# Optimization experiments

Hardware: AMD Instinct MI355X
Metric: run time of the kernel (lower is better)

Reference implementation:

```python
import jax, jax.numpy as jnp
import numpy as np

C_S, C_Z, C_H, H, PQ, PV = 384, 128, 16, 12, 4, 8
B, N = 1, 512
W_C = (2.0 / (9.0 * PQ)) ** 0.5
W_L = (1.0 / 3.0) ** 0.5
OUT_IN = H * C_Z + H * C_H + H * PV * 3 + H * PV  # 2112


def setup_inputs() -> dict:
    key = jax.random.key(0)
    ks = jax.random.split(key, 16)
    s_i = jax.random.normal(ks[0], (B, N, C_S), jnp.float32)
    z_ij = jax.random.normal(ks[1], (B, N, N, C_Z), jnp.float32)
    # random rotation matrices via QR
    raw = jax.random.normal(ks[2], (B, N, 3, 3), jnp.float32)
    q, r = jnp.linalg.qr(raw)
    rots = q * jnp.sign(jnp.diagonal(r, axis1=-2, axis2=-1))[..., None, :]
    trans = jax.random.normal(ks[3], (B, N, 3), jnp.float32)
    sc = lambda fan_in: 1.0 / np.sqrt(fan_in)
    Wq = jax.random.normal(ks[4], (C_S, H * C_H), jnp.float32) * sc(C_S)
    Wk = jax.random.normal(ks[5], (C_S, H * C_H), jnp.float32) * sc(C_S)
    Wv = jax.random.normal(ks[6], (C_S, H * C_H), jnp.float32) * sc(C_S)
    Wqp = jax.random.normal(ks[7], (C_S, H * PQ * 3), jnp.float32) * sc(C_S)
    Wkp = jax.random.normal(ks[8], (C_S, H * PQ * 3), jnp.float32) * sc(C_S)
    Wvp = jax.random.normal(ks[9], (C_S, H * PV * 3), jnp.float32) * sc(C_S)
    Wb = jax.random.normal(ks[10], (C_Z, H), jnp.float32) * sc(C_Z)
    gamma = jax.random.normal(ks[11], (1, 1, 1, H), jnp.float32)
    Wout = jax.random.normal(ks[12], (OUT_IN, C_S), jnp.float32) * sc(OUT_IN)
    bout = jnp.zeros((C_S,), jnp.float32)
    return dict(s_i=s_i, z_ij=z_ij, rots=rots, trans=trans, Wq=Wq, Wk=Wk, Wv=Wv,
                Wqp=Wqp, Wkp=Wkp, Wvp=Wvp, Wb=Wb, gamma=gamma, Wout=Wout, bout=bout)


def reference(s_i, z_ij, rots, trans, Wq, Wk, Wv, Wqp, Wkp, Wvp, Wb, gamma, Wout, bout):
    b, n = s_i.shape[0], s_i.shape[1]
    q_h = (s_i @ Wq).reshape(b, n, H, C_H)
    k_h = (s_i @ Wk).reshape(b, n, H, C_H)
    v_h = (s_i @ Wv).reshape(b, n, H, C_H)
    q_hp = (s_i @ Wqp).reshape(b, n, H, PQ, 3)
    k_hp = (s_i @ Wkp).reshape(b, n, H, PQ, 3)
    v_hp = (s_i @ Wvp).reshape(b, n, H, PV, 3)
    b_ij = z_ij @ Wb  # (b,i,j,h)

    t = trans[:, :, None, None, :]  # (b,i,1,1,3)
    apply = lambda x: jnp.einsum('bixy,bihpy->bihpx', rots, x) + t
    inv_apply = lambda x: jnp.einsum('bixy,bihpx->bihpy', rots, x - t)

    qg = apply(q_hp)  # (b,i,h,p,3) global frame
    kg = apply(k_hp)
    # pairwise rigid point distance term: (b,i,j,h)
    diff = qg[:, :, None] - kg[:, None]  # (b,i,j,h,p,3)
    dist2 = jnp.sum(diff * diff, axis=(-1, -2))

    a_s = jnp.einsum('bihd,bjhd->bijh', q_h, k_h) / (C_H ** 0.5)
    a_rigid = (W_C / 2.0) * gamma * dist2
    a = jax.nn.softmax(W_L * (a_s + b_ij - a_rigid), axis=-2)  # softmax over j

    o_hat = jnp.einsum('bijh,bijd->bihd', a, z_ij)
    o = jnp.einsum('bijh,bjhd->bihd', a, v_h)
    vg = apply(v_hp)  # (b,j,h,p,3)
    o_hp = inv_apply(jnp.einsum('bijh,bjhpx->bihpx', a, vg))  # (b,i,h,pv,3)
    o_hp_norm = jnp.sqrt(jnp.sum(o_hp * o_hp, axis=-1))  # (b,i,h,pv)

    cat = jnp.concatenate([
        o_hat.reshape(b, n, H * C_Z),
        o.reshape(b, n, H * C_H),
        o_hp.reshape(b, n, H * PV * 3),
        o_hp_norm.reshape(b, n, H * PV),
    ], axis=-1)
    return cat @ Wout + bout
```

## Files before the change

kernel.cpp:

```cpp
#include <hip/hip_runtime.h>
#include <hip/hip_bf16.h>
#include <math.h>

#define NRES 512
#define CS   384
#define CZ   128
#define NH   12
#define PW   1152
#define JB   64
#define NCH  8
#define PSTRIDE32 1040
#define KS   6
#define KAW  352

static constexpr float WL_F      = 0.57735026918962576f;
static constexpr float HALF_WC_F = 0.11785113019775792f;

typedef __attribute__((ext_vector_type(8))) short short8v;
typedef __attribute__((ext_vector_type(4))) float floatx4;

__device__ __forceinline__ ushort f2b(float f) {
    union { float f; uint u; } v; v.f = f;
    return (ushort)((v.u + 0x7FFFu + ((v.u >> 16) & 1u)) >> 16);
}
__device__ __forceinline__ float b2f(ushort b) {
    union { uint u; float f; } v; v.u = ((uint)b) << 16; return v.f;
}

__global__ __launch_bounds__(256) void k_prep(
    const float* __restrict__ Wq, const float* __restrict__ Wk,
    const float* __restrict__ Wv, const float* __restrict__ Wqp,
    const float* __restrict__ Wkp, const float* __restrict__ Wvp,
    const float* __restrict__ Wb, const float* __restrict__ Wout,
    float* __restrict__ Wcat, ushort* __restrict__ wbt16,
    ushort* __restrict__ woT)
{
    __shared__ ushort tile[64][72];
    const int bx = blockIdx.x;
    if (bx < 384) {
        const int c = bx;
        for (int col = threadIdx.x; col < PW; col += 256) {
            float v;
            if (col < 192)      v = Wq [(size_t)c * 192 + col];
            else if (col < 384) v = Wk [(size_t)c * 192 + col - 192];
            else if (col < 576) v = Wv [(size_t)c * 192 + col - 384];
            else if (col < 720) v = Wqp[(size_t)c * 144 + col - 576];
            else if (col < 864) v = Wkp[(size_t)c * 144 + col - 720];
            else                v = Wvp[(size_t)c * 288 + col - 864];
            Wcat[(size_t)c * PW + col] = v;
        }
        if (bx == 0) {
            for (int idx = threadIdx.x; idx < 16 * 128; idx += 256) {
                const int h = idx >> 7, cc = idx & 127;
                wbt16[idx] = (h < NH) ? f2b(WL_F * Wb[(size_t)cc * NH + h]) : (ushort)0;
            }
        }
    } else {
        const int t = bx - 384;
        const int k0 = (t % 33) * 64, c0 = (t / 33) * 64;
        for (int idx = threadIdx.x; idx < 4096; idx += 256) {
            const int r = idx >> 6, c = idx & 63;
            tile[r][c] = f2b(Wout[(size_t)(k0 + r) * 384 + c0 + c]);
        }
        __syncthreads();
        for (int idx = threadIdx.x; idx < 4096; idx += 256) {
            const int c = idx >> 6, r = idx & 63;
            woT[(size_t)(c0 + c) * 2112 + k0 + r] = tile[r][c];
        }
    }
}

__global__ __launch_bounds__(256) void k_gemm(
    const float* __restrict__ s, const float* __restrict__ Wcat,
    const float* __restrict__ rots, const float* __restrict__ trans,
    float* __restrict__ P)
{
    const int tid = threadIdx.x;
    const int tx = tid & 15, ty = tid >> 4;
    const int n0 = blockIdx.x * 48;
    const int m0 = blockIdx.y * 32;
    __shared__ float As[32][34];
    __shared__ float Bs[32][50];
    __shared__ float rot_lds[32][12];

    if (n0 >= 576) {
        for (int idx = tid; idx < 32 * 12; idx += 256) {
            int r = idx / 12, q = idx % 12;
            rot_lds[r][q] = (q < 9) ? rots[(size_t)(m0 + r) * 9 + q]
                                    : trans[(size_t)(m0 + r) * 3 + q - 9];
        }
    }

    float acc[2][3];
    #pragma unroll
    for (int u = 0; u < 2; ++u)
        #pragma unroll
        for (int v = 0; v < 3; ++v) acc[u][v] = 0.f;

    for (int k0 = 0; k0 < CS; k0 += 32) {
        __syncthreads();
        #pragma unroll
        for (int l = 0; l < 4; ++l) {
            int idx = tid + l * 256;
            int kk = idx & 31, r = idx >> 5;
            As[kk][r] = s[(size_t)(m0 + r) * CS + k0 + kk];
        }
        #pragma unroll
        for (int l = 0; l < 6; ++l) {
            int idx = tid + l * 256;
            int kk = idx / 48, cc = idx % 48;
            Bs[kk][cc] = Wcat[(size_t)(k0 + kk) * PW + n0 + cc];
        }
        __syncthreads();
        #pragma unroll
        for (int kk = 0; kk < 32; ++kk) {
            const float2 a = *(const float2*)&As[kk][ty * 2];
            const float b0 = Bs[kk][tx * 3], b1 = Bs[kk][tx * 3 + 1], b2 = Bs[kk][tx * 3 + 2];
            acc[0][0] += a.x * b0; acc[0][1] += a.x * b1; acc[0][2] += a.x * b2;
            acc[1][0] += a.y * b0; acc[1][1] += a.y * b1; acc[1][2] += a.y * b2;
        }
    }

    #pragma unroll
    for (int u = 0; u < 2; ++u) {
        float v0 = acc[u][0], v1 = acc[u][1], v2 = acc[u][2];
        if (n0 >= 576) {
            const float* RT = rot_lds[ty * 2 + u];
            const float p0 = v0, p1 = v1, p2 = v2;
            v0 = RT[0] * p0 + RT[1] * p1 + RT[2] * p2 + RT[9];
            v1 = RT[3] * p0 + RT[4] * p1 + RT[5] * p2 + RT[10];
            v2 = RT[6] * p0 + RT[7] * p1 + RT[8] * p2 + RT[11];
        }
        float* dst = P + (size_t)(m0 + ty * 2 + u) * PW + n0 + tx * 3;
        dst[0] = v0; dst[1] = v1; dst[2] = v2;
    }
}

__global__ __launch_bounds__(128) void k_ka(
    const float* __restrict__ P, ushort* __restrict__ Kfull)
{
    const int j = blockIdx.x;
    const int tid = threadIdx.x;
    __shared__ float njs[NH];
    const float* kr  = P + (size_t)j * PW + 192;
    const float* kgr = P + (size_t)j * PW + 720;
    if (tid < NH) {
        float s = 0.f;
        #pragma unroll
        for (int e = 0; e < 12; ++e) { const float v = kgr[tid * 12 + e]; s += v * v; }
        njs[tid] = s;
    }
    __syncthreads();
    ushort* dst = Kfull + (size_t)j * KAW;
    for (int t = tid; t < KAW; t += 128) {
        float v;
        if (t < 192)       v = kr[t];
        else if (t < 336)  v = kgr[t - 192];
        else if (t < 348)  v = njs[t - 336];
        else if (t == 348) v = 1.0f;
        else               v = 0.f;
        dst[t] = f2b(v);
    }
}

__global__ __launch_bounds__(256, 6) void k_flash(
    const float* __restrict__ z, const ushort* __restrict__ wbt16,
    const float* __restrict__ gamma, const float* __restrict__ P,
    const ushort* __restrict__ Kfull, uint* __restrict__ part)
{
    const int i   = blockIdx.x;
    const int jc  = blockIdx.y;
    const int j0  = jc * JB;
    const int tid = threadIdx.x;
    const int wid = tid >> 6, lane = tid & 63;

    __shared__ __align__(16) short zbT[128 * JB];
    __shared__ __align__(16) char  uni[10240];
    __shared__ float pm[NH], ps[NH];

    short*  BfT     = (short*)uni;
    float*  ltf     = (float*)uni;
    short*  ltb     = (short*)(uni + 4352);
    float4* halfacc = (float4*)(uni + 6400);

    uint* pb32   = part + ((size_t)i * NCH + jc) * PSTRIDE32;
    ushort* pb16 = (ushort*)pb32;
    float* pbf   = (float*)pb32;

    const int jb = wid * 16 + (lane & 15);
    const int ko = (lane >> 4) * 8;

    short8v af[4];
    {
        const float* za = z + ((size_t)i * NRES + j0 + jb) * CZ + ko;
        #pragma unroll
        for (int m = 0; m < 4; ++m) {
            const float4 f0 = *(const float4*)(za + m * 32);
            const float4 f1 = *(const float4*)(za + m * 32 + 4);
            short8v a;
            a[0] = (short)f2b(f0.x); a[1] = (short)f2b(f0.y);
            a[2] = (short)f2b(f0.z); a[3] = (short)f2b(f0.w);
            a[4] = (short)f2b(f1.x); a[5] = (short)f2b(f1.y);
            a[6] = (short)f2b(f1.z); a[7] = (short)f2b(f1.w);
            af[m] = a;
            #pragma unroll
            for (int e = 0; e < 8; ++e) {
                const int c = ko + m * 32 + e;
                zbT[c * 64 + (((jb >> 3) ^ (c & 7)) * 8) + (jb & 7)] = a[e];
            }
        }
    }
    {
        const float* prow = P + (size_t)i * PW;
        for (int t = tid; t < 12 * 352; t += 256) {
            const int h = t / 352, k = t - h * 352;
            float v = 0.f;
            if (k < 192) {
                if ((k >> 4) == h) v = 0.25f * WL_F * prow[k];
            } else if (k < 336) {
                const int e = k - 192;
                if (e / 12 == h) v = 2.f * HALF_WC_F * WL_F * gamma[h] * prow[576 + e];
            } else if (k < 348) {
                if (k - 336 == h) v = -HALF_WC_F * WL_F * gamma[h];
            } else if (k == 348) {
                float ss = 0.f;
                #pragma unroll
                for (int e = 0; e < 12; ++e) {
                    const float x = prow[576 + h * 12 + e];
                    ss += x * x;
                }
                v = -HALF_WC_F * WL_F * gamma[h] * ss;
            }
            BfT[t] = (short)f2b(v);
        }
    }
    __syncthreads();

    floatx4 lacc = {0.f, 0.f, 0.f, 0.f};
    {
        const int n  = lane & 15;
        const int nb = (n < NH) ? n : 0;
        const ushort* arow = Kfull + (size_t)(j0 + jb) * KAW + ko;
        const short*  brow = &BfT[nb * 352 + ko];
        const ushort* wrow = wbt16 + n * 128 + ko;
        #pragma unroll
        for (int st = 0; st < 11; ++st) {
            const short8v a = *(const short8v*)(arow + st * 32);
            const short8v b = *(const short8v*)(brow + st * 32);
            lacc = __builtin_amdgcn_mfma_f32_16x16x32_bf16(a, b, lacc, 0, 0, 0);
        }
        #pragma unroll
        for (int st = 0; st < 4; ++st) {
            const short8v b = *(const short8v*)(wrow + st * 32);
            lacc = __builtin_amdgcn_mfma_f32_16x16x32_bf16(af[st], b, lacc, 0, 0, 0);
        }
    }
    __syncthreads();
    {
        const int n = lane & 15;
        #pragma unroll
        for (int r = 0; r < 4; ++r)
            ltf[n * 68 + wid * 16 + (lane >> 4) * 4 + r] = lacc[r];
    }
    __syncthreads();

    if (tid < 192) {
        const int h = tid >> 4, s = tid & 15;
        float4 v = *(const float4*)&ltf[h * 68 + s * 4];
        float m = fmaxf(fmaxf(v.x, v.y), fmaxf(v.z, v.w));
        #pragma unroll
        for (int o = 1; o < 16; o <<= 1) m = fmaxf(m, __shfl_xor(m, o));
        float4 e;
        e.x = __expf(v.x - m); e.y = __expf(v.y - m);
        e.z = __expf(v.z - m); e.w = __expf(v.w - m);
        float sum = e.x + e.y + e.z + e.w;
        #pragma unroll
        for (int o = 1; o < 16; o <<= 1) sum += __shfl_xor(sum, o);
        *(float4*)&ltf[h * 68 + s * 4] = e;
        const uint lo = (uint)f2b(e.x) | ((uint)f2b(e.y) << 16);
        const uint hi = (uint)f2b(e.z) | ((uint)f2b(e.w) << 16);
        uint* dst = (uint*)&ltb[h * 64 + (((s >> 1) ^ (h & 7)) * 8) + (s & 1) * 4];
        dst[0] = lo; dst[1] = hi;
        if (s == 0) { pm[h] = m; ps[h] = sum; }
    } else {
        const int tt = tid - 192;
        uint* dst = (uint*)&ltb[(12 + (tt >> 4)) * 64 + (tt & 15) * 4];
        dst[0] = 0u; dst[1] = 0u;
    }
    __syncthreads();

    {
        const int hrow = lane & 15;
        const int u0 = (lane >> 4), u1 = u0 + 4;
        const short8v a0 = *(const short8v*)&ltb[hrow * 64 + ((u0 ^ (hrow & 7)) * 8)];
        const short8v a1 = *(const short8v*)&ltb[hrow * 64 + ((u1 ^ (hrow & 7)) * 8)];
        #pragma unroll
        for (int t = 0; t < 2; ++t) {
            const int d = (wid * 2 + t) * 16 + (lane & 15);
            const short8v b0 = *(const short8v*)&zbT[d * 64 + ((u0 ^ (d & 7)) * 8)];
            const short8v b1 = *(const short8v*)&zbT[d * 64 + ((u1 ^ (d & 7)) * 8)];
            floatx4 acc = {0.f, 0.f, 0.f, 0.f};
            acc = __builtin_amdgcn_mfma_f32_16x16x32_bf16(a0, b0, acc, 0, 0, 0);
            acc = __builtin_amdgcn_mfma_f32_16x16x32_bf16(a1, b1, acc, 0, 0, 0);
            #pragma unroll
            for (int r = 0; r < 4; ++r) {
                const int h = u0 * 4 + r;
                if (h < NH) pb16[h * 128 + d] = f2b(acc[r]);
            }
        }
    }

    {
        if (tid < 240) {
            const int half = tid / 120, col = tid % 120;
            int h;
            const float* base;
            if (col < 48) { h = col >> 2;               base = P + (size_t)j0 * PW + 384 + col * 4; }
            else          { const int cc = col - 48; h = cc / 6; base = P + (size_t)j0 * PW + 864 + cc * 4; }
            base += (size_t)(half * 32) * PW;
            const float* er = &ltf[h * 68 + half * 32];
            float ax = 0.f, ay = 0.f, az = 0.f, aw = 0.f;
            #pragma unroll 4
            for (int jj = 0; jj < 32; ++jj) {
                const float e = er[jj];
                const float4 v = *(const float4*)(base + (size_t)jj * PW);
                ax += e * v.x; ay += e * v.y; az += e * v.z; aw += e * v.w;
            }
            halfacc[tid] = make_float4(ax, ay, az, aw);
        }
        __syncthreads();
        if (tid < 120) {
            const float4 s0 = halfacc[tid], s1 = halfacc[tid + 120];
            const int off16 = (tid < 48) ? 1536 + tid * 4 : 1728 + (tid - 48) * 4;
            uint* dst = (uint*)&pb16[off16];
            dst[0] = (uint)f2b(s0.x + s1.x) | ((uint)f2b(s0.y + s1.y) << 16);
            dst[1] = (uint)f2b(s0.z + s1.z) | ((uint)f2b(s0.w + s1.w) << 16);
        }
        if (tid < NH) { pbf[1008 + tid] = pm[tid]; pbf[1020 + tid] = ps[tid]; }
    }
}

__global__ __launch_bounds__(256) void k_combine(
    const uint* __restrict__ part, const float* __restrict__ rots,
    const float* __restrict__ trans, ushort* __restrict__ cat16)
{
    const int i   = blockIdx.x;
    const int tid = threadIdx.x;
    __shared__ float wgt[NCH][NH];
    __shared__ float ohp[288];

    const uint* base = part + (size_t)i * NCH * PSTRIDE32;
    if (tid < NH) {
        const int h = tid;
        float mm[NCH];
        float M = -1e30f;
        #pragma unroll
        for (int c = 0; c < NCH; ++c) {
            mm[c] = ((const float*)(base + c * PSTRIDE32))[1008 + h];
            M = fmaxf(M, mm[c]);
        }
        float S = 0.f;
        #pragma unroll
        for (int c = 0; c < NCH; ++c) {
            const float w = __expf(mm[c] - M);
            S += w * ((const float*)(base + c * PSTRIDE32))[1020 + h];
            wgt[c][h] = w;
        }
        const float inv = 1.0f / S;
        #pragma unroll
        for (int c = 0; c < NCH; ++c) wgt[c][h] *= inv;
    }
    __syncthreads();

    ushort* crow = cat16 + (size_t)i * 2112;
    uint*   crowu = (uint*)crow;
    for (int idx2 = tid; idx2 < 768; idx2 += 256) {
        const int h = idx2 >> 6;
        float v0 = 0.f, v1 = 0.f;
        #pragma unroll
        for (int c = 0; c < NCH; ++c) {
            const uint u = base[c * PSTRIDE32 + idx2];
            const float w = wgt[c][h];
            v0 += b2f((ushort)u) * w;
            v1 += b2f((ushort)(u >> 16)) * w;
        }
        crowu[idx2] = (uint)f2b(v0) | ((uint)f2b(v1) << 16);
    }
    if (tid < 96) {
        const int h = tid >> 3;
        float v0 = 0.f, v1 = 0.f;
        #pragma unroll
        for (int c = 0; c < NCH; ++c) {
            const uint u = base[c * PSTRIDE32 + 768 + tid];
            const float w = wgt[c][h];
            v0 += b2f((ushort)u) * w;
            v1 += b2f((ushort)(u >> 16)) * w;
        }
        crowu[768 + tid] = (uint)f2b(v0) | ((uint)f2b(v1) << 16);
    }
    if (tid < 144) {
        const int h = tid / 12;
        float v0 = 0.f, v1 = 0.f;
        #pragma unroll
        for (int c = 0; c < NCH; ++c) {
            const uint u = base[c * PSTRIDE32 + 864 + tid];
            const float w = wgt[c][h];
            v0 += b2f((ushort)u) * w;
            v1 += b2f((ushort)(u >> 16)) * w;
        }
        ohp[tid * 2] = v0; ohp[tid * 2 + 1] = v1;
    }
    __syncthreads();

    if (tid < 96) {
        const int h = tid >> 3, p = tid & 7;
        float R[9];
        #pragma unroll
        for (int k = 0; k < 9; ++k) R[k] = rots[(size_t)i * 9 + k];
        const float g0 = ohp[h * 24 + p * 3 + 0] - trans[(size_t)i * 3 + 0];
        const float g1 = ohp[h * 24 + p * 3 + 1] - trans[(size_t)i * 3 + 1];
        const float g2 = ohp[h * 24 + p * 3 + 2] - trans[(size_t)i * 3 + 2];
        const float oy0 = R[0] * g0 + R[3] * g1 + R[6] * g2;
        const float oy1 = R[1] * g0 + R[4] * g1 + R[7] * g2;
        const float oy2 = R[2] * g0 + R[5] * g1 + R[8] * g2;
        crow[1728 + h * 24 + p * 3 + 0] = f2b(oy0);
        crow[1728 + h * 24 + p * 3 + 1] = f2b(oy1);
        crow[1728 + h * 24 + p * 3 + 2] = f2b(oy2);
        crow[2016 + h * 8 + p] = f2b(sqrtf(oy0 * oy0 + oy1 * oy1 + oy2 * oy2));
    }
}

__global__ __launch_bounds__(256) void k_out(
    const ushort* __restrict__ cat16, const ushort* __restrict__ woT,
    float* __restrict__ opart)
{
    const int tid = threadIdx.x;
    const int wid = tid >> 6, lane = tid & 63;
    const int wm = wid >> 1, wn = wid & 1;
    const int i0 = blockIdx.x * 32 + wm * 16;
    const int c0 = blockIdx.y * 32 + wn * 16;
    const int k0 = blockIdx.z * 352;
    const ushort* arow = cat16 + (size_t)(i0 + (lane & 15)) * 2112 + k0 + (lane >> 4) * 8;
    const ushort* brow = woT   + (size_t)(c0 + (lane & 15)) * 2112 + k0 + (lane >> 4) * 8;
    floatx4 acc = {0.f, 0.f, 0.f, 0.f};
    #pragma unroll
    for (int st = 0; st < 11; ++st) {
        const short8v a = *(const short8v*)(arow + st * 32);
        const short8v b = *(const short8v*)(brow + st * 32);
        acc = __builtin_amdgcn_mfma_f32_16x16x32_bf16(a, b, acc, 0, 0, 0);
    }
    float* ob = opart + (size_t)blockIdx.z * 512 * 384;
    #pragma unroll
    for (int r = 0; r < 4; ++r) {
        const int i = i0 + (lane >> 4) * 4 + r;
        ob[(size_t)i * 384 + c0 + (lane & 15)] = acc[r];
    }
}

__global__ __launch_bounds__(256) void k_outred(
    const float* __restrict__ opart, const float* __restrict__ bout,
    float* __restrict__ out)
{
    const int e4 = blockIdx.x * 256 + threadIdx.x;
    const float4* p = (const float4*)opart;
    const float4 b = ((const float4*)bout)[e4 % 96];
    float4 r = b;
    #pragma unroll
    for (int k = 0; k < KS; ++k) {
        const float4 v = p[e4 + k * 49152];
        r.x += v.x; r.y += v.y; r.z += v.z; r.w += v.w;
    }
    ((float4*)out)[e4] = r;
}

extern "C" void kernel_launch(void* const* d_in, const int* in_sizes, int n_in,
                              void* d_out, int out_size, void* d_ws, size_t ws_size,
                              hipStream_t stream)
{
    const float* s_i   = (const float*)d_in[0];
    const float* z_ij  = (const float*)d_in[1];
    const float* rots  = (const float*)d_in[2];
    const float* trans = (const float*)d_in[3];
    const float* Wq    = (const float*)d_in[4];
    const float* Wk    = (const float*)d_in[5];
    const float* Wv    = (const float*)d_in[6];
    const float* Wqp   = (const float*)d_in[7];
    const float* Wkp   = (const float*)d_in[8];
    const float* Wvp   = (const float*)d_in[9];
    const float* Wb    = (const float*)d_in[10];
    const float* gamma = (const float*)d_in[11];
    const float* Wout  = (const float*)d_in[12];
    const float* bout  = (const float*)d_in[13];
    float* ws = (float*)d_ws;
    float*  wcat  = ws;
    float*  P     = ws + 442368;
    uint*   part  = (uint*)(P + 589824);
    float*  opart = (float*)part;
    ushort* cat16 = (ushort*)(part + (size_t)512 * NCH * PSTRIDE32);
    ushort* wbt16 = cat16 + 1081344;
    ushort* kfull = wbt16 + 2048;
    ushort* woT   = kfull + 512 * KAW;
    float*  out   = (float*)d_out;

    hipLaunchKernelGGL(k_prep, dim3(582), dim3(256), 0, stream,
                       Wq, Wk, Wv, Wqp, Wkp, Wvp, Wb, Wout, wcat, wbt16, woT);
    hipLaunchKernelGGL(k_gemm, dim3(24, 16), dim3(256), 0, stream,
                       s_i, wcat, rots, trans, P);
    hipLaunchKernelGGL(k_ka, dim3(512), dim3(128), 0, stream, P, kfull);
    hipLaunchKernelGGL(k_flash, dim3(512, NCH), dim3(256), 0, stream,
                       z_ij, wbt16, gamma, P, kfull, part);
    hipLaunchKernelGGL(k_combine, dim3(512), dim3(256), 0, stream,
                       part, rots, trans, cat16);
    hipLaunchKernelGGL(k_out, dim3(16, 12, KS), dim3(256), 0, stream,
                       cat16, woT, opart);
    hipLaunchKernelGGL(k_outred, dim3(192), dim3(256), 0, stream,
                       opart, bout, out);
}
```

Before: 125.3 us.

## Precompute per-row query B-matrix in k_ka and shrink k_flash LDS footprint

The per-residue query operand (BfT, 12x352 bf16), which was rebuilt in LDS by each of the 8 j-chunk blocks of k_flash, is now built once per row in k_ka and written to a global Bfull buffer. k_flash reads B fragments straight from global memory, drops the BfT staging loop and one barrier, reuses zbT as scratch for halfacc, writes softmax max and sum directly to the partials, and raises the launch-bounds occupancy hint from 6 to 7. Bfull shares workspace with cat16, which is written later by k_combine. In exchange k_flash does more global (likely cache-hit) loads, and the lower LDS use is meant to allow more resident blocks.

```diff
diff --git a/kernel.cpp b/kernel.cpp
--- a/kernel.cpp
+++ b/kernel.cpp
@@ -12,6 +12,7 @@
 #define PSTRIDE32 1040
 #define KS   6
 #define KAW  352
+#define BFW  4224
 
 static constexpr float WL_F      = 0.57735026918962576f;
 static constexpr float HALF_WC_F = 0.11785113019775792f;
@@ -137,21 +138,28 @@
 }
 
 __global__ __launch_bounds__(128) void k_ka(
-    const float* __restrict__ P, ushort* __restrict__ Kfull)
-{
-    const int j = blockIdx.x;
+    const float* __restrict__ P, const float* __restrict__ gamma,
+    ushort* __restrict__ Kfull, ushort* __restrict__ Bfull)
+{
+    const int r = blockIdx.x;
     const int tid = threadIdx.x;
     __shared__ float njs[NH];
-    const float* kr  = P + (size_t)j * PW + 192;
-    const float* kgr = P + (size_t)j * PW + 720;
+    __shared__ float nqs[NH];
+    const float* prow = P + (size_t)r * PW;
+    const float* kr   = prow + 192;
+    const float* qgr  = prow + 576;
+    const float* kgr  = prow + 720;
     if (tid < NH) {
-        float s = 0.f;
-        #pragma unroll
-        for (int e = 0; e < 12; ++e) { const float v = kgr[tid * 12 + e]; s += v * v; }
-        njs[tid] = s;
+        float s = 0.f, sq = 0.f;
+        #pragma unroll
+        for (int e = 0; e < 12; ++e) {
+            const float v = kgr[tid * 12 + e];  s += v * v;
+            const float q = qgr[tid * 12 + e];  sq += q * q;
+        }
+        njs[tid] = s; nqs[tid] = sq;
     }
     __syncthreads();
-    ushort* dst = Kfull + (size_t)j * KAW;
+    ushort* dst = Kfull + (size_t)r * KAW;
     for (int t = tid; t < KAW; t += 128) {
         float v;
         if (t < 192)       v = kr[t];
@@ -161,12 +169,28 @@
         else               v = 0.f;
         dst[t] = f2b(v);
     }
-}
-
-__global__ __launch_bounds__(256, 6) void k_flash(
+    ushort* bd = Bfull + (size_t)r * BFW;
+    for (int t = tid; t < BFW; t += 128) {
+        const int h = t / 352, k = t - h * 352;
+        float v = 0.f;
+        if (k < 192) {
+            if ((k >> 4) == h) v = 0.25f * WL_F * prow[k];
+        } else if (k < 336) {
+            const int e = k - 192;
+            if (e / 12 == h) v = 2.f * HALF_WC_F * WL_F * gamma[h] * qgr[e];
+        } else if (k < 348) {
+            if (k - 336 == h) v = -HALF_WC_F * WL_F * gamma[h];
+        } else if (k == 348) {
+            v = -HALF_WC_F * WL_F * gamma[h] * nqs[h];
+        }
+        bd[t] = f2b(v);
+    }
+}
+
+__global__ __launch_bounds__(256, 7) void k_flash(
     const float* __restrict__ z, const ushort* __restrict__ wbt16,
-    const float* __restrict__ gamma, const float* __restrict__ P,
-    const ushort* __restrict__ Kfull, uint* __restrict__ part)
+    const float* __restrict__ P, const ushort* __restrict__ Kfull,
+    const ushort* __restrict__ Bfull, uint* __restrict__ part)
 {
     const int i   = blockIdx.x;
     const int jc  = blockIdx.y;
@@ -175,13 +199,9 @@
     const int wid = tid >> 6, lane = tid & 63;
 
     __shared__ __align__(16) short zbT[128 * JB];
-    __shared__ __align__(16) char  uni[10240];
-    __shared__ float pm[NH], ps[NH];
-
-    short*  BfT     = (short*)uni;
-    float*  ltf     = (float*)uni;
-    short*  ltb     = (short*)(uni + 4352);
-    float4* halfacc = (float4*)(uni + 6400);
+    __shared__ __align__(16) float ltf[12 * 68];
+    __shared__ __align__(16) short ltb[16 * 64];
+    float4* halfacc = (float4*)zbT;
 
     uint* pb32   = part + ((size_t)i * NCH + jc) * PSTRIDE32;
     ushort* pb16 = (ushort*)pb32;
@@ -210,39 +230,14 @@
             }
         }
     }
-    {
-        const float* prow = P + (size_t)i * PW;
-        for (int t = tid; t < 12 * 352; t += 256) {
-            const int h = t / 352, k = t - h * 352;
-            float v = 0.f;
-            if (k < 192) {
-                if ((k >> 4) == h) v = 0.25f * WL_F * prow[k];
-            } else if (k < 336) {
-                const int e = k - 192;
-                if (e / 12 == h) v = 2.f * HALF_WC_F * WL_F * gamma[h] * prow[576 + e];
-            } else if (k < 348) {
-                if (k - 336 == h) v = -HALF_WC_F * WL_F * gamma[h];
-            } else if (k == 348) {
-                float ss = 0.f;
-                #pragma unroll
-                for (int e = 0; e < 12; ++e) {
-                    const float x = prow[576 + h * 12 + e];
-                    ss += x * x;
-                }
-                v = -HALF_WC_F * WL_F * gamma[h] * ss;
-            }
-            BfT[t] = (short)f2b(v);
-        }
-    }
-    __syncthreads();
-
-    floatx4 lacc = {0.f, 0.f, 0.f, 0.f};
+
     {
         const int n  = lane & 15;
         const int nb = (n < NH) ? n : 0;
         const ushort* arow = Kfull + (size_t)(j0 + jb) * KAW + ko;
-        const short*  brow = &BfT[nb * 352 + ko];
+        const ushort* brow = Bfull + (size_t)i * BFW + nb * 352 + ko;
         const ushort* wrow = wbt16 + n * 128 + ko;
+        floatx4 lacc = {0.f, 0.f, 0.f, 0.f};
         #pragma unroll
         for (int st = 0; st < 11; ++st) {
             const short8v a = *(const short8v*)(arow + st * 32);
@@ -254,13 +249,11 @@
             const short8v b = *(const short8v*)(wrow + st * 32);
             lacc = __builtin_amdgcn_mfma_f32_16x16x32_bf16(af[st], b, lacc, 0, 0, 0);
         }
-    }
-    __syncthreads();
-    {
-        const int n = lane & 15;
-        #pragma unroll
-        for (int r = 0; r < 4; ++r)
-            ltf[n * 68 + wid * 16 + (lane >> 4) * 4 + r] = lacc[r];
+        if (n < NH) {
+            #pragma unroll
+            for (int r = 0; r < 4; ++r)
+                ltf[n * 68 + wid * 16 + (lane >> 4) * 4 + r] = lacc[r];
+        }
     }
     __syncthreads();
 
@@ -281,7 +274,7 @@
         const uint hi = (uint)f2b(e.z) | ((uint)f2b(e.w) << 16);
         uint* dst = (uint*)&ltb[h * 64 + (((s >> 1) ^ (h & 7)) * 8) + (s & 1) * 4];
         dst[0] = lo; dst[1] = hi;
-        if (s == 0) { pm[h] = m; ps[h] = sum; }
+        if (s == 0) { pbf[1008 + h] = m; pbf[1020 + h] = sum; }
     } else {
         const int tt = tid - 192;
         uint* dst = (uint*)&ltb[(12 + (tt >> 4)) * 64 + (tt & 15) * 4];
@@ -309,6 +302,7 @@
             }
         }
     }
+    __syncthreads();
 
     {
         if (tid < 240) {
@@ -336,7 +330,6 @@
             dst[0] = (uint)f2b(s0.x + s1.x) | ((uint)f2b(s0.y + s1.y) << 16);
             dst[1] = (uint)f2b(s0.z + s1.z) | ((uint)f2b(s0.w + s1.w) << 16);
         }
-        if (tid < NH) { pbf[1008 + tid] = pm[tid]; pbf[1020 + tid] = ps[tid]; }
     }
 }
 
@@ -496,8 +489,9 @@
     float*  P     = ws + 442368;
     uint*   part  = (uint*)(P + 589824);
     float*  opart = (float*)part;
-    ushort* cat16 = (ushort*)(part + (size_t)512 * NCH * PSTRIDE32);
-    ushort* wbt16 = cat16 + 1081344;
+    ushort* bfull = (ushort*)(part + (size_t)512 * NCH * PSTRIDE32);
+    ushort* cat16 = bfull;
+    ushort* wbt16 = bfull + (size_t)512 * BFW;
     ushort* kfull = wbt16 + 2048;
     ushort* woT   = kfull + 512 * KAW;
     float*  out   = (float*)d_out;
@@ -506,9 +500,10 @@
                        Wq, Wk, Wv, Wqp, Wkp, Wvp, Wb, Wout, wcat, wbt16, woT);
     hipLaunchKernelGGL(k_gemm, dim3(24, 16), dim3(256), 0, stream,
                        s_i, wcat, rots, trans, P);
-    hipLaunchKernelGGL(k_ka, dim3(512), dim3(128), 0, stream, P, kfull);
+    hipLaunchKernelGGL(k_ka, dim3(512), dim3(128), 0, stream,
+                       P, gamma, kfull, bfull);
     hipLaunchKernelGGL(k_flash, dim3(512, NCH), dim3(256), 0, stream,
-                       z_ij, wbt16, gamma, P, kfull, part);
+                       z_ij, wbt16, P, kfull, bfull, part);
     hipLaunchKernelGGL(k_combine, dim3(512), dim3(256), 0, stream,
                        part, rots, trans, cat16);
     hipLaunchKernelGGL(k_out, dim3(16, 12, KS), dim3(256), 0, stream,
```

Result: slower. 132.1 us (+5.4%).
